# Kernel optimization log

Measured on AMD Instinct MI355X. Metric: run time of the kernel, lower is better.

## Reference

```python
import jax, jax.numpy as jnp
import numpy as np

N_NODES = 100000
E = 1000000
IN_DIM = 64
HID = 64


def setup_inputs() -> dict:
    key = jax.random.key(0)
    ks = jax.random.split(key, 8)
    edge_emb = jax.random.normal(ks[0], (E, IN_DIM), dtype=jnp.float32)
    edge_indices = jax.random.randint(ks[1], (E, 2), 0, N_NODES, dtype=jnp.int64)
    s_in = 1.0 / np.sqrt(IN_DIM)
    s_h = 1.0 / np.sqrt(HID)
    Wf = jax.random.uniform(ks[2], (IN_DIM, HID), minval=-s_in, maxval=s_in, dtype=jnp.float32)
    bf = jax.random.uniform(ks[3], (HID,), minval=-s_in, maxval=s_in, dtype=jnp.float32)
    Wb = jax.random.uniform(ks[4], (IN_DIM, HID), minval=-s_in, maxval=s_in, dtype=jnp.float32)
    bb = jax.random.uniform(ks[5], (HID,), minval=-s_in, maxval=s_in, dtype=jnp.float32)
    Wg = jax.random.uniform(ks[6], (HID, 1), minval=-s_h, maxval=s_h, dtype=jnp.float32)
    bg = jax.random.uniform(ks[7], (1,), minval=-s_h, maxval=s_h, dtype=jnp.float32)
    return {"edge_emb": edge_emb, "Wf": Wf, "bf": bf, "Wb": Wb, "bb": bb,
            "Wg": Wg, "bg": bg, "edge_indices": edge_indices}


def reference(edge_emb, Wf, bf, Wb, bb, Wg, bg, edge_indices):
    u = edge_indices[:, 0]
    v = edge_indices[:, 1]
    # node_to_edges derived from incidence: sum of incident edge embeddings + degree
    node_sum = (jax.ops.segment_sum(edge_emb, u, num_segments=N_NODES)
                + jax.ops.segment_sum(edge_emb, v, num_segments=N_NODES))  # [N, d]
    ones = jnp.ones((edge_emb.shape[0],), edge_emb.dtype)
    deg = (jax.ops.segment_sum(ones, u, num_segments=N_NODES)
           + jax.ops.segment_sum(ones, v, num_segments=N_NODES))  # [N]

    def excl_mean(n):
        # mean over the node's incident edges excluding the current edge;
        # zeros when the current edge is the node's only incident edge.
        d = deg[n]                              # [E]
        s = node_sum[n] - edge_emb              # [E, d_in]
        denom = jnp.maximum(d - 1.0, 1.0)[:, None]
        return jnp.where((d > 1.0)[:, None], s / denom, jnp.zeros_like(s))

    agg_u = excl_mean(u)
    agg_v = excl_mean(v)
    agg_forward = agg_u @ Wf + bf               # [E, H]
    agg_backward = agg_v @ Wb + bb              # [E, H]
    gate = jax.nn.sigmoid((agg_forward + agg_backward) @ Wg + bg)  # [E, 1]
    return gate * agg_forward + (1.0 - gate) * agg_backward
```

## Files before the change

kernel.cpp:

```cpp
#include <hip/hip_runtime.h>
#include <hip/hip_bf16.h>
#include <math.h>

#define N_NODES 100000
#define DIM 64
#define BATCH 16
#define LDS_PITCH 72

typedef __attribute__((ext_vector_type(8))) short short8;
typedef __attribute__((ext_vector_type(4))) float floatx4;

__device__ __forceinline__ short f2bf(float x) {
    unsigned u = __float_as_uint(x);
    u += 0x7FFF + ((u >> 16) & 1);
    return (short)(u >> 16);
}
__device__ __forceinline__ float bf2f(unsigned short b) {
    return __uint_as_float(((unsigned)b) << 16);
}

__global__ __launch_bounds__(256) void scatter_kernel(
    const float* __restrict__ edge_emb, const int* __restrict__ idx,
    __hip_bfloat162* __restrict__ node_sum, float* __restrict__ deg, int n_edges)
{
    long long gid = (long long)blockIdx.x * blockDim.x + threadIdx.x;
    if (gid >= (long long)n_edges * 32) return;
    int e = (int)(gid >> 5);
    int p = (int)(gid & 31);
    float2 ev = ((const float2*)edge_emb)[gid];
    int2 uv = ((const int2*)idx)[e];
    union { unsigned u32; __hip_bfloat162 h; } cv;
    cv.u32 = (unsigned)(unsigned short)f2bf(ev.x)
           | ((unsigned)(unsigned short)f2bf(ev.y) << 16);
    unsafeAtomicAdd(&node_sum[(size_t)uv.x * 32 + p], cv.h);
    unsafeAtomicAdd(&node_sum[(size_t)uv.y * 32 + p], cv.h);
    if (p == 0) {
        unsafeAtomicAdd(&deg[uv.x], 1.f);
        unsafeAtomicAdd(&deg[uv.y], 1.f);
    }
}

__global__ __launch_bounds__(256) void bucket_fill_kernel(
    const int* __restrict__ idx, unsigned* __restrict__ cnt,
    unsigned* __restrict__ bucket, int cap, int n_edges)
{
    int e = blockIdx.x * 256 + threadIdx.x;
    if (e >= n_edges) return;
    int2 uv = ((const int2*)idx)[e];
    unsigned pu = atomicAdd(&cnt[uv.x], 1u);
    if (pu < (unsigned)cap) bucket[(size_t)uv.x * cap + pu] = (unsigned)e;
    unsigned pv = atomicAdd(&cnt[uv.y], 1u);
    if (pv < (unsigned)cap) bucket[(size_t)uv.y * cap + pv] = (unsigned)e;
}

__global__ __launch_bounds__(256) void gather_sum_kernel(
    const float* __restrict__ edge_emb, const unsigned* __restrict__ bucket,
    const unsigned* __restrict__ cnt, unsigned short* __restrict__ node_sum,
    float* __restrict__ degf, int cap)
{
    const int lane = threadIdx.x & 63;
    const int wslot = threadIdx.x >> 6;
    const int nwaves = gridDim.x * 4;
    for (int n = blockIdx.x * 4 + wslot; n < N_NODES; n += nwaves) {
        unsigned c = cnt[n];
        if (c > (unsigned)cap) c = (unsigned)cap;
        const unsigned* bptr = bucket + (size_t)n * cap;
        float acc0 = 0.f, acc1 = 0.f, acc2 = 0.f, acc3 = 0.f;
        for (unsigned base = 0; base < c; base += 64) {
            int cc = (int)(c - base); if (cc > 64) cc = 64;
            unsigned bv = (lane < cc) ? bptr[base + lane] : 0u;
            int j = 0;
            for (; j + 3 < cc; j += 4) {
                unsigned e0 = (unsigned)__shfl((int)bv, j);
                unsigned e1 = (unsigned)__shfl((int)bv, j + 1);
                unsigned e2 = (unsigned)__shfl((int)bv, j + 2);
                unsigned e3 = (unsigned)__shfl((int)bv, j + 3);
                acc0 += edge_emb[(size_t)e0 * 64 + lane];
                acc1 += edge_emb[(size_t)e1 * 64 + lane];
                acc2 += edge_emb[(size_t)e2 * 64 + lane];
                acc3 += edge_emb[(size_t)e3 * 64 + lane];
            }
            for (; j < cc; ++j) {
                unsigned e0 = (unsigned)__shfl((int)bv, j);
                acc0 += edge_emb[(size_t)e0 * 64 + lane];
            }
        }
        node_sum[(size_t)n * 64 + lane] = (unsigned short)f2bf((acc0 + acc1) + (acc2 + acc3));
        if (lane == 0) degf[n] = (float)c;
    }
}

__global__ __launch_bounds__(256) void fused_edge_kernel(
    const float* __restrict__ edge_emb,
    const int* __restrict__ idx,
    const unsigned short* __restrict__ node_sum,
    const float* __restrict__ deg,
    const float* __restrict__ Wf, const float* __restrict__ bf,
    const float* __restrict__ Wb, const float* __restrict__ bb,
    const float* __restrict__ Wg, const float* __restrict__ bg,
    float* __restrict__ out, int n_edges)
{
    __shared__ short lds[4][2][BATCH * LDS_PITCH];
    const int lane = threadIdx.x & 63;
    const int l15 = lane & 15;
    const int q = lane >> 4;
    const int wslot = threadIdx.x >> 6;
    const int wid = __builtin_amdgcn_readfirstlane(blockIdx.x * 4 + wslot);
    const int nwaves = gridDim.x * 4;

    short8 bWf[4][2], bWb[4][2];
#pragma unroll
    for (int nt = 0; nt < 4; ++nt)
#pragma unroll
        for (int kt = 0; kt < 2; ++kt) {
            short8 f, g;
#pragma unroll
            for (int j = 0; j < 8; ++j) {
                int k = kt * 32 + q * 8 + j;
                int n = nt * 16 + l15;
                f[j] = f2bf(Wf[k * 64 + n]);
                g[j] = f2bf(Wb[k * 64 + n]);
            }
            bWf[nt][kt] = f;
            bWb[nt][kt] = g;
        }
    float bfv[4], bbv[4], wgv[4];
#pragma unroll
    for (int nt = 0; nt < 4; ++nt) {
        bfv[nt] = bf[nt * 16 + l15];
        bbv[nt] = bb[nt * 16 + l15];
        wgv[nt] = Wg[nt * 16 + l15];
    }
    const float bgv = bg[0];

    short* ldsU = lds[wslot][0];
    short* ldsV = lds[wslot][1];

    const int nbatches = n_edges / BATCH;
    for (int b = wid; b < nbatches; b += nwaves) {
        const int e0 = b * BATCH;
#pragma unroll
        for (int i = 0; i < BATCH; ++i) {
            const int e = e0 + i;
            const int u = idx[2 * e];
            const int v = idx[2 * e + 1];
            const float du = deg[u];
            const float dv = deg[v];
            const float invu = (du > 1.f) ? 1.f / (du - 1.f) : 0.f;
            const float invv = (dv > 1.f) ? 1.f / (dv - 1.f) : 0.f;
            const float ev = edge_emb[(size_t)e * 64 + lane];
            const float nsu = bf2f(node_sum[(size_t)u * 64 + lane]);
            const float nsv = bf2f(node_sum[(size_t)v * 64 + lane]);
            ldsU[i * LDS_PITCH + lane] = f2bf((nsu - ev) * invu);
            ldsV[i * LDS_PITCH + lane] = f2bf((nsv - ev) * invv);
        }

        short8 aU[2], aV[2];
#pragma unroll
        for (int kt = 0; kt < 2; ++kt) {
            const int off = l15 * LDS_PITCH + kt * 32 + q * 8;
            aU[kt] = *(const short8*)&ldsU[off];
            aV[kt] = *(const short8*)&ldsV[off];
        }

        floatx4 cU[4], cV[4];
#pragma unroll
        for (int nt = 0; nt < 4; ++nt) {
            floatx4 z = {0.f, 0.f, 0.f, 0.f};
            z = __builtin_amdgcn_mfma_f32_16x16x32_bf16(aU[0], bWf[nt][0], z, 0, 0, 0);
            cU[nt] = __builtin_amdgcn_mfma_f32_16x16x32_bf16(aU[1], bWf[nt][1], z, 0, 0, 0);
            floatx4 z2 = {0.f, 0.f, 0.f, 0.f};
            z2 = __builtin_amdgcn_mfma_f32_16x16x32_bf16(aV[0], bWb[nt][0], z2, 0, 0, 0);
            cV[nt] = __builtin_amdgcn_mfma_f32_16x16x32_bf16(aV[1], bWb[nt][1], z2, 0, 0, 0);
        }

        float p[4] = {0.f, 0.f, 0.f, 0.f};
#pragma unroll
        for (int nt = 0; nt < 4; ++nt)
#pragma unroll
            for (int r = 0; r < 4; ++r) {
                float af = cU[nt][r] + bfv[nt];
                float ab = cV[nt][r] + bbv[nt];
                cU[nt][r] = af;
                cV[nt][r] = ab;
                p[r] = fmaf(af + ab, wgv[nt], p[r]);
            }
#pragma unroll
        for (int r = 0; r < 4; ++r) {
            float s = p[r];
            s += __shfl_xor(s, 1);
            s += __shfl_xor(s, 2);
            s += __shfl_xor(s, 4);
            s += __shfl_xor(s, 8);
            p[r] = 1.f / (1.f + __expf(-(s + bgv)));
        }
#pragma unroll
        for (int nt = 0; nt < 4; ++nt)
#pragma unroll
            for (int r = 0; r < 4; ++r) {
                const int e = e0 + q * 4 + r;
                out[(size_t)e * 64 + nt * 16 + l15] =
                    fmaf(p[r], cU[nt][r] - cV[nt][r], cV[nt][r]);
            }
    }
}

extern "C" void kernel_launch(void* const* d_in, const int* in_sizes, int n_in,
                              void* d_out, int out_size, void* d_ws, size_t ws_size,
                              hipStream_t stream) {
    const float* edge_emb = (const float*)d_in[0];
    const float* Wf = (const float*)d_in[1];
    const float* bf = (const float*)d_in[2];
    const float* Wb = (const float*)d_in[3];
    const float* bb = (const float*)d_in[4];
    const float* Wg = (const float*)d_in[5];
    const float* bg = (const float*)d_in[6];
    const int* idx = (const int*)d_in[7];
    float* out = (float*)d_out;

    const int n_edges = in_sizes[7] / 2;

    char* ws = (char*)d_ws;
    const size_t ns_bytes  = (size_t)N_NODES * DIM * 2;
    const size_t deg_bytes = (size_t)N_NODES * 4;
    const size_t cnt_bytes = (size_t)N_NODES * 4;
    unsigned short* node_sum = (unsigned short*)ws;
    float* deg = (float*)(ws + ns_bytes);
    unsigned* cnt = (unsigned*)(ws + ns_bytes + deg_bytes);
    unsigned* bucket = (unsigned*)(ws + ns_bytes + deg_bytes + cnt_bytes);
    const size_t fixed_bytes = ns_bytes + deg_bytes + cnt_bytes;

    int cap = 0;
    if (ws_size >= fixed_bytes + (size_t)N_NODES * 128 * 4)      cap = 128;
    else if (ws_size >= fixed_bytes + (size_t)N_NODES * 64 * 4)  cap = 64;

    if (cap) {
        hipMemsetAsync(cnt, 0, cnt_bytes, stream);
        int blocksF = (n_edges + 255) / 256;
        bucket_fill_kernel<<<blocksF, 256, 0, stream>>>(idx, cnt, bucket, cap, n_edges);
        gather_sum_kernel<<<2048, 256, 0, stream>>>(edge_emb, bucket, cnt,
                                                    node_sum, deg, cap);
    } else {
        hipMemsetAsync(d_ws, 0, ns_bytes + deg_bytes, stream);
        long long sthreads = (long long)n_edges * 32;
        int blocks1 = (int)((sthreads + 255) / 256);
        scatter_kernel<<<blocks1, 256, 0, stream>>>(edge_emb, idx,
            (__hip_bfloat162*)node_sum, deg, n_edges);
    }

    int blocks2 = 2048;
    fused_edge_kernel<<<blocks2, 256, 0, stream>>>(
        edge_emb, idx, node_sum, deg,
        Wf, bf, Wb, bb, Wg, bg, out, n_edges);
}
```

Baseline: 879.3 us.

## Vectorize gather-sum over quarter-waves and load MFMA A operands directly from global

The gather-sum kernel now handles four nodes per wave, each 16-lane group reading float4 rows with software-prefetched bucket indices instead of broadcasting indices through shuffles. The fused edge kernel builds the MFMA A fragments straight from vectorized global loads of node_sum and edge_emb in the fragment layout, removing the per-edge scalar loads and the LDS staging round trip. The weight B fragments move from registers to LDS, shared by the block, with a launch-bounds occupancy hint. This aims to cut load instruction count and raise occupancy, at the cost of extra LDS reads per MFMA and less lane coalescing per row.

Result: faster. 747.3 us (-15.0%).

```diff
diff --git a/kernel.cpp b/kernel.cpp
--- a/kernel.cpp
+++ b/kernel.cpp
@@ -5,10 +5,10 @@
 #define N_NODES 100000
 #define DIM 64
 #define BATCH 16
-#define LDS_PITCH 72
 
 typedef __attribute__((ext_vector_type(8))) short short8;
 typedef __attribute__((ext_vector_type(4))) float floatx4;
+typedef __attribute__((ext_vector_type(4))) unsigned short us4;
 
 __device__ __forceinline__ short f2bf(float x) {
     unsigned u = __float_as_uint(x);
@@ -59,38 +59,64 @@
     float* __restrict__ degf, int cap)
 {
     const int lane = threadIdx.x & 63;
+    const int g = lane >> 4;
+    const int c16 = lane & 15;
     const int wslot = threadIdx.x >> 6;
-    const int nwaves = gridDim.x * 4;
-    for (int n = blockIdx.x * 4 + wslot; n < N_NODES; n += nwaves) {
+    const int slot0 = (blockIdx.x * 4 + wslot) * 4 + g;
+    const int nslots = gridDim.x * 16;
+    const float4* emb4 = (const float4*)edge_emb;
+
+    for (int n = slot0; n < N_NODES; n += nslots) {
         unsigned c = cnt[n];
         if (c > (unsigned)cap) c = (unsigned)cap;
         const unsigned* bptr = bucket + (size_t)n * cap;
-        float acc0 = 0.f, acc1 = 0.f, acc2 = 0.f, acc3 = 0.f;
-        for (unsigned base = 0; base < c; base += 64) {
-            int cc = (int)(c - base); if (cc > 64) cc = 64;
-            unsigned bv = (lane < cc) ? bptr[base + lane] : 0u;
-            int j = 0;
-            for (; j + 3 < cc; j += 4) {
-                unsigned e0 = (unsigned)__shfl((int)bv, j);
-                unsigned e1 = (unsigned)__shfl((int)bv, j + 1);
-                unsigned e2 = (unsigned)__shfl((int)bv, j + 2);
-                unsigned e3 = (unsigned)__shfl((int)bv, j + 3);
-                acc0 += edge_emb[(size_t)e0 * 64 + lane];
-                acc1 += edge_emb[(size_t)e1 * 64 + lane];
-                acc2 += edge_emb[(size_t)e2 * 64 + lane];
-                acc3 += edge_emb[(size_t)e3 * 64 + lane];
-            }
-            for (; j < cc; ++j) {
-                unsigned e0 = (unsigned)__shfl((int)bv, j);
-                acc0 += edge_emb[(size_t)e0 * 64 + lane];
-            }
-        }
-        node_sum[(size_t)n * 64 + lane] = (unsigned short)f2bf((acc0 + acc1) + (acc2 + acc3));
-        if (lane == 0) degf[n] = (float)c;
-    }
-}
-
-__global__ __launch_bounds__(256) void fused_edge_kernel(
+        float4 a0 = {0,0,0,0}, a1 = {0,0,0,0}, a2 = {0,0,0,0}, a3 = {0,0,0,0};
+        unsigned j = 0;
+        unsigned id0 = 0, id1 = 0, id2 = 0, id3 = 0;
+        if (c >= 4) { id0 = bptr[0]; id1 = bptr[1]; id2 = bptr[2]; id3 = bptr[3]; }
+        for (; j + 8 <= c; j += 4) {
+            unsigned n0 = bptr[j+4], n1 = bptr[j+5], n2 = bptr[j+6], n3 = bptr[j+7];
+            float4 v0 = emb4[(size_t)id0 * 16 + c16];
+            float4 v1 = emb4[(size_t)id1 * 16 + c16];
+            float4 v2 = emb4[(size_t)id2 * 16 + c16];
+            float4 v3 = emb4[(size_t)id3 * 16 + c16];
+            a0.x += v0.x; a0.y += v0.y; a0.z += v0.z; a0.w += v0.w;
+            a1.x += v1.x; a1.y += v1.y; a1.z += v1.z; a1.w += v1.w;
+            a2.x += v2.x; a2.y += v2.y; a2.z += v2.z; a2.w += v2.w;
+            a3.x += v3.x; a3.y += v3.y; a3.z += v3.z; a3.w += v3.w;
+            id0 = n0; id1 = n1; id2 = n2; id3 = n3;
+        }
+        if (j + 4 <= c) {
+            float4 v0 = emb4[(size_t)id0 * 16 + c16];
+            float4 v1 = emb4[(size_t)id1 * 16 + c16];
+            float4 v2 = emb4[(size_t)id2 * 16 + c16];
+            float4 v3 = emb4[(size_t)id3 * 16 + c16];
+            a0.x += v0.x; a0.y += v0.y; a0.z += v0.z; a0.w += v0.w;
+            a1.x += v1.x; a1.y += v1.y; a1.z += v1.z; a1.w += v1.w;
+            a2.x += v2.x; a2.y += v2.y; a2.z += v2.z; a2.w += v2.w;
+            a3.x += v3.x; a3.y += v3.y; a3.z += v3.z; a3.w += v3.w;
+            j += 4;
+        }
+        for (; j < c; ++j) {
+            unsigned e0 = bptr[j];
+            float4 v0 = emb4[(size_t)e0 * 16 + c16];
+            a0.x += v0.x; a0.y += v0.y; a0.z += v0.z; a0.w += v0.w;
+        }
+        float sx = (a0.x + a1.x) + (a2.x + a3.x);
+        float sy = (a0.y + a1.y) + (a2.y + a3.y);
+        float sz = (a0.z + a1.z) + (a2.z + a3.z);
+        float sw = (a0.w + a1.w) + (a2.w + a3.w);
+        us4 o;
+        o[0] = (unsigned short)f2bf(sx);
+        o[1] = (unsigned short)f2bf(sy);
+        o[2] = (unsigned short)f2bf(sz);
+        o[3] = (unsigned short)f2bf(sw);
+        *(us4*)&node_sum[(size_t)n * 64 + c16 * 4] = o;
+        if (c16 == 0) degf[n] = (float)c;
+    }
+}
+
+__global__ __launch_bounds__(256, 4) void fused_edge_kernel(
     const float* __restrict__ edge_emb,
     const int* __restrict__ idx,
     const unsigned short* __restrict__ node_sum,
@@ -100,30 +126,23 @@
     const float* __restrict__ Wg, const float* __restrict__ bg,
     float* __restrict__ out, int n_edges)
 {
-    __shared__ short lds[4][2][BATCH * LDS_PITCH];
+    __shared__ __align__(16) short ldsB[16][64 * 8];
     const int lane = threadIdx.x & 63;
     const int l15 = lane & 15;
     const int q = lane >> 4;
     const int wslot = threadIdx.x >> 6;
-    const int wid = __builtin_amdgcn_readfirstlane(blockIdx.x * 4 + wslot);
-    const int nwaves = gridDim.x * 4;
-
-    short8 bWf[4][2], bWb[4][2];
-#pragma unroll
-    for (int nt = 0; nt < 4; ++nt)
-#pragma unroll
-        for (int kt = 0; kt < 2; ++kt) {
-            short8 f, g;
-#pragma unroll
-            for (int j = 0; j < 8; ++j) {
-                int k = kt * 32 + q * 8 + j;
-                int n = nt * 16 + l15;
-                f[j] = f2bf(Wf[k * 64 + n]);
-                g[j] = f2bf(Wb[k * 64 + n]);
-            }
-            bWf[nt][kt] = f;
-            bWb[nt][kt] = g;
-        }
+
+    for (int f = wslot; f < 16; f += 4) {
+        const float* W = (f < 8) ? Wf : Wb;
+        const int nt = (f >> 1) & 3, kt = f & 1;
+        short8 w;
+#pragma unroll
+        for (int j = 0; j < 8; ++j)
+            w[j] = f2bf(W[(kt * 32 + q * 8 + j) * 64 + nt * 16 + l15]);
+        *(short8*)&ldsB[f][lane * 8] = w;
+    }
+    __syncthreads();
+
     float bfv[4], bbv[4], wgv[4];
 #pragma unroll
     for (int nt = 0; nt < 4; ++nt) {
@@ -133,45 +152,63 @@
     }
     const float bgv = bg[0];
 
-    short* ldsU = lds[wslot][0];
-    short* ldsV = lds[wslot][1];
-
+    const int wid = __builtin_amdgcn_readfirstlane(blockIdx.x * 4 + wslot);
+    const int nwaves = gridDim.x * 4;
     const int nbatches = n_edges / BATCH;
+
     for (int b = wid; b < nbatches; b += nwaves) {
         const int e0 = b * BATCH;
-#pragma unroll
-        for (int i = 0; i < BATCH; ++i) {
-            const int e = e0 + i;
-            const int u = idx[2 * e];
-            const int v = idx[2 * e + 1];
-            const float du = deg[u];
-            const float dv = deg[v];
-            const float invu = (du > 1.f) ? 1.f / (du - 1.f) : 0.f;
-            const float invv = (dv > 1.f) ? 1.f / (dv - 1.f) : 0.f;
-            const float ev = edge_emb[(size_t)e * 64 + lane];
-            const float nsu = bf2f(node_sum[(size_t)u * 64 + lane]);
-            const float nsv = bf2f(node_sum[(size_t)v * 64 + lane]);
-            ldsU[i * LDS_PITCH + lane] = f2bf((nsu - ev) * invu);
-            ldsV[i * LDS_PITCH + lane] = f2bf((nsv - ev) * invv);
-        }
+        const int e = e0 + l15;
+        const int2 uv = ((const int2*)idx)[e];
+        const float du = deg[uv.x];
+        const float dv = deg[uv.y];
+        const float invu = (du > 1.f) ? 1.f / (du - 1.f) : 0.f;
+        const float invv = (dv > 1.f) ? 1.f / (dv - 1.f) : 0.f;
+        const float4* eb = (const float4*)(edge_emb + (size_t)e * 64 + q * 8);
+        const unsigned short* nsu = node_sum + (size_t)uv.x * 64 + q * 8;
+        const unsigned short* nsv = node_sum + (size_t)uv.y * 64 + q * 8;
 
         short8 aU[2], aV[2];
 #pragma unroll
         for (int kt = 0; kt < 2; ++kt) {
-            const int off = l15 * LDS_PITCH + kt * 32 + q * 8;
-            aU[kt] = *(const short8*)&ldsU[off];
-            aV[kt] = *(const short8*)&ldsV[off];
+            const float4 m0 = eb[kt * 8];
+            const float4 m1 = eb[kt * 8 + 1];
+            const uint4 su = *(const uint4*)(nsu + kt * 32);
+            const uint4 sv = *(const uint4*)(nsv + kt * 32);
+            short8 au, av;
+            au[0] = f2bf((__uint_as_float(su.x << 16)          - m0.x) * invu);
+            au[1] = f2bf((__uint_as_float(su.x & 0xffff0000u)  - m0.y) * invu);
+            au[2] = f2bf((__uint_as_float(su.y << 16)          - m0.z) * invu);
+            au[3] = f2bf((__uint_as_float(su.y & 0xffff0000u)  - m0.w) * invu);
+            au[4] = f2bf((__uint_as_float(su.z << 16)          - m1.x) * invu);
+            au[5] = f2bf((__uint_as_float(su.z & 0xffff0000u)  - m1.y) * invu);
+            au[6] = f2bf((__uint_as_float(su.w << 16)          - m1.z) * invu);
+            au[7] = f2bf((__uint_as_float(su.w & 0xffff0000u)  - m1.w) * invu);
+            av[0] = f2bf((__uint_as_float(sv.x << 16)          - m0.x) * invv);
+            av[1] = f2bf((__uint_as_float(sv.x & 0xffff0000u)  - m0.y) * invv);
+            av[2] = f2bf((__uint_as_float(sv.y << 16)          - m0.z) * invv);
+            av[3] = f2bf((__uint_as_float(sv.y & 0xffff0000u)  - m0.w) * invv);
+            av[4] = f2bf((__uint_as_float(sv.z << 16)          - m1.x) * invv);
+            av[5] = f2bf((__uint_as_float(sv.z & 0xffff0000u)  - m1.y) * invv);
+            av[6] = f2bf((__uint_as_float(sv.w << 16)          - m1.z) * invv);
+            av[7] = f2bf((__uint_as_float(sv.w & 0xffff0000u)  - m1.w) * invv);
+            aU[kt] = au;
+            aV[kt] = av;
         }
 
         floatx4 cU[4], cV[4];
 #pragma unroll
         for (int nt = 0; nt < 4; ++nt) {
+            const short8 b0 = *(const short8*)&ldsB[nt * 2 + 0][lane * 8];
+            const short8 b1 = *(const short8*)&ldsB[nt * 2 + 1][lane * 8];
+            const short8 g0 = *(const short8*)&ldsB[8 + nt * 2 + 0][lane * 8];
+            const short8 g1 = *(const short8*)&ldsB[8 + nt * 2 + 1][lane * 8];
             floatx4 z = {0.f, 0.f, 0.f, 0.f};
-            z = __builtin_amdgcn_mfma_f32_16x16x32_bf16(aU[0], bWf[nt][0], z, 0, 0, 0);
-            cU[nt] = __builtin_amdgcn_mfma_f32_16x16x32_bf16(aU[1], bWf[nt][1], z, 0, 0, 0);
+            z = __builtin_amdgcn_mfma_f32_16x16x32_bf16(aU[0], b0, z, 0, 0, 0);
+            cU[nt] = __builtin_amdgcn_mfma_f32_16x16x32_bf16(aU[1], b1, z, 0, 0, 0);
             floatx4 z2 = {0.f, 0.f, 0.f, 0.f};
-            z2 = __builtin_amdgcn_mfma_f32_16x16x32_bf16(aV[0], bWb[nt][0], z2, 0, 0, 0);
-            cV[nt] = __builtin_amdgcn_mfma_f32_16x16x32_bf16(aV[1], bWb[nt][1], z2, 0, 0, 0);
+            z2 = __builtin_amdgcn_mfma_f32_16x16x32_bf16(aV[0], g0, z2, 0, 0, 0);
+            cV[nt] = __builtin_amdgcn_mfma_f32_16x16x32_bf16(aV[1], g1, z2, 0, 0, 0);
         }
 
         float p[4] = {0.f, 0.f, 0.f, 0.f};
@@ -198,8 +235,8 @@
         for (int nt = 0; nt < 4; ++nt)
 #pragma unroll
             for (int r = 0; r < 4; ++r) {
-                const int e = e0 + q * 4 + r;
-                out[(size_t)e * 64 + nt * 16 + l15] =
+                const int eo = e0 + q * 4 + r;
+                out[(size_t)eo * 64 + nt * 16 + l15] =
                     fmaf(p[r], cU[nt][r] - cV[nt][r], cV[nt][r]);
             }
     }
```
